# Kernel tuning notes

Hardware: AMD Instinct MI355X
Metric: run time of the kernel (lower is better)

## Reference

```python
import jax, jax.numpy as jnp
import numpy as np

B, T, C, H = 256, 256, 384, 64  # batch, seq (== block_size), n_embd, head_size


def setup_inputs() -> dict:
    key = jax.random.key(0)
    kx, kk, kq, kv = jax.random.split(key, 4)
    scale = C ** -0.5
    x = jax.random.normal(kx, (B, T, C), dtype=jnp.float32)
    Wk = jax.random.normal(kk, (C, H), dtype=jnp.float32) * scale
    Wq = jax.random.normal(kq, (C, H), dtype=jnp.float32) * scale
    Wv = jax.random.normal(kv, (C, H), dtype=jnp.float32) * scale
    return {"x": x, "Wk": Wk, "Wq": Wq, "Wv": Wv}


def reference(x, Wk, Wq, Wv):
    # Single causal self-attention head (x_kv=None path). Dropout is eval-mode (identity).
    Tn = x.shape[1]
    k = x @ Wk            # [B, T, H]
    q = x @ Wq            # [B, T, H]
    v = x @ Wv            # [B, T, H]
    inv_sqrt_d = k.shape[-1] ** -0.5
    wei = jnp.einsum('bth,bsh->bts', q, k) * inv_sqrt_d  # [B, T, T]
    causal = jnp.tril(jnp.ones((Tn, Tn), dtype=bool))
    wei = jnp.where(causal, wei, -jnp.inf)
    wei = jax.nn.softmax(wei, axis=-1)
    out = jnp.einsum('bts,bsh->bth', wei, v)             # [B, T, H]
    return out
```

## Files before the change

### kernel.cpp

```cpp
#include <hip/hip_runtime.h>

#define BATCH 256
#define SEQ   256
#define CDIM  384
#define HDIM  64

typedef __attribute__((ext_vector_type(8))) short bf16x8;
typedef __attribute__((ext_vector_type(4))) float f32x4;

__device__ __forceinline__ unsigned f2bf(float f) {
  union { float f; unsigned u; } v; v.f = f;
  unsigned r = v.u + 0x7FFFu + ((v.u >> 16) & 1u);
  return r >> 16;
}

__global__ void wtrans_kernel(const float* __restrict__ Wk, const float* __restrict__ Wq,
                              const float* __restrict__ Wv, unsigned short* __restrict__ WTf) {
  int gid = blockIdx.x * 256 + threadIdx.x;
  if (gid >= 192 * CDIM) return;
  int n = gid / CDIM, kk = gid - n * CDIM;
  const float* W = (n < 64) ? Wq : (n < 128) ? Wk : Wv;
  int nt = n >> 4, ln = n & 15, ks = kk >> 5, sub = (kk >> 3) & 3, j = kk & 7;
  int lane = ln + 16 * sub;
  WTf[(((size_t)ks * 12 + nt) * 64 + lane) * 8 + j] =
      (unsigned short)f2bf(W[kk * HDIM + (n & 63)]);
}

__global__ __launch_bounds__(512, 2) void proj_kernel(
    const float* __restrict__ x, const unsigned short* __restrict__ WTf,
    unsigned short* __restrict__ qws, unsigned short* __restrict__ kws,
    unsigned short* __restrict__ vT) {
  __shared__ unsigned short wtlds[73728];
  __shared__ unsigned short vtile[64][72];
  const int tid = threadIdx.x, bid = blockIdx.x;
  const int w = tid >> 6, lane = tid & 63;
  const int ln15 = lane & 15, quad = lane >> 4;

  {
    const uint4* src = (const uint4*)WTf;
    uint4* dst = (uint4*)wtlds;
    #pragma unroll
    for (int i = 0; i < 18; ++i) dst[i * 512 + tid] = src[i * 512 + tid];
  }

  const int t0 = bid * 128 + w * 16;
  const float* xrow = x + (size_t)(t0 + ln15) * CDIM + quad * 8;
  bf16x8 bx[12];
  #pragma unroll
  for (int hh = 0; hh < 2; ++hh) {
    float4 A[12];
    #pragma unroll
    for (int j = 0; j < 6; ++j) {
      A[2 * j]     = *(const float4*)(xrow + (hh * 6 + j) * 32);
      A[2 * j + 1] = *(const float4*)(xrow + (hh * 6 + j) * 32 + 4);
    }
    #pragma unroll
    for (int j = 0; j < 6; ++j) {
      bf16x8 t;
      t[0] = (short)f2bf(A[2 * j].x);     t[1] = (short)f2bf(A[2 * j].y);
      t[2] = (short)f2bf(A[2 * j].z);     t[3] = (short)f2bf(A[2 * j].w);
      t[4] = (short)f2bf(A[2 * j + 1].x); t[5] = (short)f2bf(A[2 * j + 1].y);
      t[6] = (short)f2bf(A[2 * j + 1].z); t[7] = (short)f2bf(A[2 * j + 1].w);
      bx[hh * 6 + j] = t;
    }
  }

  __syncthreads();

  f32x4 acc[12];
  #pragma unroll
  for (int nt = 0; nt < 12; ++nt) acc[nt] = (f32x4){0.f, 0.f, 0.f, 0.f};

  #pragma unroll
  for (int ks = 0; ks < 12; ++ks) {
    #pragma unroll
    for (int nt = 0; nt < 12; ++nt) {
      bf16x8 aw = *(const bf16x8*)&wtlds[((ks * 12 + nt) * 64 + lane) * 8];
      acc[nt] = __builtin_amdgcn_mfma_f32_16x16x32_bf16(aw, bx[ks], acc[nt], 0, 0, 0);
    }
  }

  #pragma unroll
  for (int nt = 0; nt < 8; ++nt) {
    unsigned p0 = f2bf(acc[nt][0]) | (f2bf(acc[nt][1]) << 16);
    unsigned p1 = f2bf(acc[nt][2]) | (f2bf(acc[nt][3]) << 16);
    int hl = (nt & 3) * 16 + quad * 4;
    unsigned short* dst = (nt < 4) ? qws : kws;
    *(uint2*)&dst[(size_t)(t0 + ln15) * HDIM + hl] = (uint2){p0, p1};
  }

  #pragma unroll
  for (int p = 0; p < 2; ++p) {
    if ((w >> 2) == p) {
      int tl = (w & 3) * 16 + ln15;
      #pragma unroll
      for (int nt = 8; nt < 12; ++nt) {
        int hl = (nt & 3) * 16 + quad * 4;
        #pragma unroll
        for (int i = 0; i < 4; ++i)
          vtile[hl + i][tl] = (unsigned short)f2bf(acc[nt][i]);
      }
    }
    __syncthreads();
    {
      int h = tid >> 3, c = tid & 7;
      uint4 d = *(const uint4*)&vtile[h][c * 8];
      *(uint4*)&vT[((size_t)(bid >> 1) * 64 + h) * SEQ + (bid & 1) * 128 + p * 64 + c * 8] = d;
    }
    __syncthreads();
  }
}

__global__ __launch_bounds__(512, 4) void attn_kernel(
    const unsigned short* __restrict__ qws, const unsigned short* __restrict__ kws,
    const unsigned short* __restrict__ vT, float* __restrict__ out) {
  __shared__ unsigned short kl[256][72];
  __shared__ unsigned short vt[64][264];
  __shared__ unsigned short pl[8][16][36];
  const int tid = threadIdx.x;
  const int b = blockIdx.x >> 1, hgrp = blockIdx.x & 1;
  const int w = tid >> 6, lane = tid & 63;
  const int ln15 = lane & 15, quad = lane >> 4;

  for (int c = tid; c < 2048; c += 512) {
    int t = c >> 3, hc = c & 7;
    *(uint4*)&kl[t][hc * 8] = *(const uint4*)&kws[(size_t)(b * 256 + t) * HDIM + hc * 8];
  }
  for (int c = tid; c < 2048; c += 512) {
    int hh = c >> 5, tc = c & 31;
    *(uint4*)&vt[hh][tc * 8] = *(const uint4*)&vT[(size_t)(b * 64 + hh) * SEQ + tc * 8];
  }
  __syncthreads();

  const int mt = 4 * (w >> 1) + (hgrp ? (1 + (w & 1)) : (3 * (w & 1)));
  const int t0 = mt * 16;
  const int NT = (mt | 1) + 1;

  bf16x8 aq[2];
  #pragma unroll
  for (int ks = 0; ks < 2; ++ks)
    aq[ks] = *(const bf16x8*)&qws[(size_t)(b * 256 + t0 + ln15) * HDIM + ks * 32 + quad * 8];

  float sv[16][4];
  #pragma unroll
  for (int nt = 0; nt < 16; ++nt) {
    if (nt < NT) {
      f32x4 acc = (f32x4){0.f, 0.f, 0.f, 0.f};
      #pragma unroll
      for (int ks = 0; ks < 2; ++ks) {
        bf16x8 bf = *(const bf16x8*)&kl[nt * 16 + ln15][ks * 32 + quad * 8];
        acc = __builtin_amdgcn_mfma_f32_16x16x32_bf16(aq[ks], bf, acc, 0, 0, 0);
      }
      int colg = nt * 16 + ln15;
      #pragma unroll
      for (int i = 0; i < 4; ++i) {
        int rowg = t0 + quad * 4 + i;
        sv[nt][i] = (colg <= rowg) ? acc[i] * 0.125f : -3.0e38f;
      }
    }
  }
  float mx[4] = {-3.0e38f, -3.0e38f, -3.0e38f, -3.0e38f};
  #pragma unroll
  for (int nt = 0; nt < 16; ++nt)
    if (nt < NT) {
      #pragma unroll
      for (int i = 0; i < 4; ++i) mx[i] = fmaxf(mx[i], sv[nt][i]);
    }
  #pragma unroll
  for (int i = 0; i < 4; ++i) {
    mx[i] = fmaxf(mx[i], __shfl_xor(mx[i], 8, 64));
    mx[i] = fmaxf(mx[i], __shfl_xor(mx[i], 4, 64));
    mx[i] = fmaxf(mx[i], __shfl_xor(mx[i], 2, 64));
    mx[i] = fmaxf(mx[i], __shfl_xor(mx[i], 1, 64));
  }
  float sm[4] = {0.f, 0.f, 0.f, 0.f};
  #pragma unroll
  for (int nt = 0; nt < 16; ++nt)
    if (nt < NT) {
      #pragma unroll
      for (int i = 0; i < 4; ++i) {
        float e = __expf(sv[nt][i] - mx[i]);
        sv[nt][i] = e;
        sm[i] += e;
      }
    }
  #pragma unroll
  for (int i = 0; i < 4; ++i) {
    sm[i] += __shfl_xor(sm[i], 8, 64);
    sm[i] += __shfl_xor(sm[i], 4, 64);
    sm[i] += __shfl_xor(sm[i], 2, 64);
    sm[i] += __shfl_xor(sm[i], 1, 64);
  }
  float inv[4];
  #pragma unroll
  for (int i = 0; i < 4; ++i) inv[i] = 1.0f / sm[i];

  f32x4 o[4];
  #pragma unroll
  for (int ont = 0; ont < 4; ++ont) o[ont] = (f32x4){0.f, 0.f, 0.f, 0.f};

  for (int kc = 0; kc < 8; ++kc) {
    if (kc * 2 < NT) {
      #pragma unroll
      for (int half = 0; half < 2; ++half) {
        int nt = kc * 2 + half;
        #pragma unroll
        for (int i = 0; i < 4; ++i)
          pl[w][quad * 4 + i][half * 16 + ln15] =
              (unsigned short)f2bf(sv[nt][i] * inv[i]);
      }
      bf16x8 pa = *(const bf16x8*)&pl[w][ln15][quad * 8];
      #pragma unroll
      for (int ont = 0; ont < 4; ++ont) {
        bf16x8 vb = *(const bf16x8*)&vt[ont * 16 + ln15][kc * 32 + quad * 8];
        o[ont] = __builtin_amdgcn_mfma_f32_16x16x32_bf16(pa, vb, o[ont], 0, 0, 0);
      }
    }
  }

  #pragma unroll
  for (int ont = 0; ont < 4; ++ont) {
    int h = ont * 16 + ln15;
    #pragma unroll
    for (int i = 0; i < 4; ++i)
      out[(size_t)(b * 256 + t0 + quad * 4 + i) * HDIM + h] = o[ont][i];
  }
}

extern "C" void kernel_launch(void* const* d_in, const int* in_sizes, int n_in,
                              void* d_out, int out_size, void* d_ws, size_t ws_size,
                              hipStream_t stream) {
  const float* x  = (const float*)d_in[0];
  const float* Wk = (const float*)d_in[1];
  const float* Wq = (const float*)d_in[2];
  const float* Wv = (const float*)d_in[3];
  float* out = (float*)d_out;

  char* ws = (char*)d_ws;
  unsigned short* WTf = (unsigned short*)ws;
  unsigned short* qws = (unsigned short*)(ws + 262144);
  unsigned short* kws = qws + (size_t)BATCH * SEQ * HDIM;
  unsigned short* vT  = kws + (size_t)BATCH * SEQ * HDIM;

  wtrans_kernel<<<(192 * CDIM + 255) / 256, 256, 0, stream>>>(Wk, Wq, Wv, WTf);
  proj_kernel<<<512, 512, 0, stream>>>(x, WTf, qws, kws, vT);
  attn_kernel<<<2 * BATCH, 512, 0, stream>>>(qws, kws, vT, out);
}
```

Before: 182.5 us.

## Fuse QKV projection and causal attention into one per-batch kernel

Merges the projection and attention kernels into one kernel with one block per batch. Each block computes Q, K and V for all 256 rows into shared memory, reusing the weight LDS region, then runs causal attention with each wave handling a short and a long row tile to balance the work. This removes the global round trip for bf16 Q/K/V and one kernel launch. In exchange the grid shrinks to 256 blocks, which risks lower occupancy and less latency hiding on a GPU with many CUs.

Result: slower. 190.0 us (+4.1%).

```diff
diff --git a/kernel.cpp b/kernel.cpp
--- a/kernel.cpp
+++ b/kernel.cpp
@@ -26,204 +26,196 @@
       (unsigned short)f2bf(W[kk * HDIM + (n & 63)]);
 }
 
-__global__ __launch_bounds__(512, 2) void proj_kernel(
+__global__ __launch_bounds__(512, 2) void fused_kernel(
     const float* __restrict__ x, const unsigned short* __restrict__ WTf,
-    unsigned short* __restrict__ qws, unsigned short* __restrict__ kws,
-    unsigned short* __restrict__ vT) {
-  __shared__ unsigned short wtlds[73728];
-  __shared__ unsigned short vtile[64][72];
-  const int tid = threadIdx.x, bid = blockIdx.x;
+    float* __restrict__ out) {
+  __shared__ unsigned short lds[73728];
+  const int tid = threadIdx.x, b = blockIdx.x;
   const int w = tid >> 6, lane = tid & 63;
   const int ln15 = lane & 15, quad = lane >> 4;
 
   {
     const uint4* src = (const uint4*)WTf;
-    uint4* dst = (uint4*)wtlds;
+    uint4* dst = (uint4*)lds;
     #pragma unroll
     for (int i = 0; i < 18; ++i) dst[i * 512 + tid] = src[i * 512 + tid];
   }
 
-  const int t0 = bid * 128 + w * 16;
-  const float* xrow = x + (size_t)(t0 + ln15) * CDIM + quad * 8;
-  bf16x8 bx[12];
+  bf16x8 bx[2][12];
+  {
+    const float* xr0 = x + (size_t)(b * 256 + w * 32 + ln15) * CDIM + quad * 8;
+    #pragma unroll
+    for (int rg = 0; rg < 2; ++rg) {
+      const float* xr = xr0 + rg * 16 * CDIM;
+      #pragma unroll
+      for (int hh = 0; hh < 2; ++hh) {
+        float4 A[12];
+        #pragma unroll
+        for (int j = 0; j < 6; ++j) {
+          A[2 * j]     = *(const float4*)(xr + (hh * 6 + j) * 32);
+          A[2 * j + 1] = *(const float4*)(xr + (hh * 6 + j) * 32 + 4);
+        }
+        #pragma unroll
+        for (int j = 0; j < 6; ++j) {
+          bf16x8 t;
+          t[0] = (short)f2bf(A[2 * j].x);     t[1] = (short)f2bf(A[2 * j].y);
+          t[2] = (short)f2bf(A[2 * j].z);     t[3] = (short)f2bf(A[2 * j].w);
+          t[4] = (short)f2bf(A[2 * j + 1].x); t[5] = (short)f2bf(A[2 * j + 1].y);
+          t[6] = (short)f2bf(A[2 * j + 1].z); t[7] = (short)f2bf(A[2 * j + 1].w);
+          bx[rg][hh * 6 + j] = t;
+        }
+      }
+    }
+  }
+
+  __syncthreads();
+
+  f32x4 acc[2][12];
   #pragma unroll
-  for (int hh = 0; hh < 2; ++hh) {
-    float4 A[12];
-    #pragma unroll
-    for (int j = 0; j < 6; ++j) {
-      A[2 * j]     = *(const float4*)(xrow + (hh * 6 + j) * 32);
-      A[2 * j + 1] = *(const float4*)(xrow + (hh * 6 + j) * 32 + 4);
-    }
-    #pragma unroll
-    for (int j = 0; j < 6; ++j) {
-      bf16x8 t;
-      t[0] = (short)f2bf(A[2 * j].x);     t[1] = (short)f2bf(A[2 * j].y);
-      t[2] = (short)f2bf(A[2 * j].z);     t[3] = (short)f2bf(A[2 * j].w);
-      t[4] = (short)f2bf(A[2 * j + 1].x); t[5] = (short)f2bf(A[2 * j + 1].y);
-      t[6] = (short)f2bf(A[2 * j + 1].z); t[7] = (short)f2bf(A[2 * j + 1].w);
-      bx[hh * 6 + j] = t;
-    }
-  }
-
-  __syncthreads();
-
-  f32x4 acc[12];
-  #pragma unroll
-  for (int nt = 0; nt < 12; ++nt) acc[nt] = (f32x4){0.f, 0.f, 0.f, 0.f};
+  for (int rg = 0; rg < 2; ++rg)
+    #pragma unroll
+    for (int nt = 0; nt < 12; ++nt) acc[rg][nt] = (f32x4){0.f, 0.f, 0.f, 0.f};
 
   #pragma unroll
   for (int ks = 0; ks < 12; ++ks) {
     #pragma unroll
     for (int nt = 0; nt < 12; ++nt) {
-      bf16x8 aw = *(const bf16x8*)&wtlds[((ks * 12 + nt) * 64 + lane) * 8];
-      acc[nt] = __builtin_amdgcn_mfma_f32_16x16x32_bf16(aw, bx[ks], acc[nt], 0, 0, 0);
-    }
-  }
+      bf16x8 aw = *(const bf16x8*)&lds[((ks * 12 + nt) * 64 + lane) * 8];
+      acc[0][nt] = __builtin_amdgcn_mfma_f32_16x16x32_bf16(aw, bx[0][ks], acc[0][nt], 0, 0, 0);
+      acc[1][nt] = __builtin_amdgcn_mfma_f32_16x16x32_bf16(aw, bx[1][ks], acc[1][nt], 0, 0, 0);
+    }
+  }
+
+  __syncthreads();
+
+  unsigned short (*QL)[72]  = (unsigned short(*)[72])lds;
+  unsigned short (*KL)[72]  = (unsigned short(*)[72])(lds + 18432);
+  unsigned short (*VT)[264] = (unsigned short(*)[264])(lds + 36864);
+  unsigned short (*PL)[36]  = (unsigned short(*)[36])(lds + 53760 + w * 576);
 
   #pragma unroll
-  for (int nt = 0; nt < 8; ++nt) {
-    unsigned p0 = f2bf(acc[nt][0]) | (f2bf(acc[nt][1]) << 16);
-    unsigned p1 = f2bf(acc[nt][2]) | (f2bf(acc[nt][3]) << 16);
-    int hl = (nt & 3) * 16 + quad * 4;
-    unsigned short* dst = (nt < 4) ? qws : kws;
-    *(uint2*)&dst[(size_t)(t0 + ln15) * HDIM + hl] = (uint2){p0, p1};
-  }
-
-  #pragma unroll
-  for (int p = 0; p < 2; ++p) {
-    if ((w >> 2) == p) {
-      int tl = (w & 3) * 16 + ln15;
+  for (int rg = 0; rg < 2; ++rg) {
+    const int trow = w * 32 + rg * 16 + ln15;
+    #pragma unroll
+    for (int nt = 0; nt < 4; ++nt) {
+      f32x4 a = acc[rg][nt];
+      unsigned p0 = f2bf(a[0]) | (f2bf(a[1]) << 16);
+      unsigned p1 = f2bf(a[2]) | (f2bf(a[3]) << 16);
+      *(uint2*)&QL[trow][nt * 16 + quad * 4] = (uint2){p0, p1};
+    }
+    #pragma unroll
+    for (int nt = 4; nt < 8; ++nt) {
+      f32x4 a = acc[rg][nt];
+      unsigned p0 = f2bf(a[0]) | (f2bf(a[1]) << 16);
+      unsigned p1 = f2bf(a[2]) | (f2bf(a[3]) << 16);
+      *(uint2*)&KL[trow][(nt - 4) * 16 + quad * 4] = (uint2){p0, p1};
+    }
+    #pragma unroll
+    for (int nt = 8; nt < 12; ++nt) {
+      f32x4 a = acc[rg][nt];
+      const int h = (nt - 8) * 16 + quad * 4;
       #pragma unroll
-      for (int nt = 8; nt < 12; ++nt) {
-        int hl = (nt & 3) * 16 + quad * 4;
-        #pragma unroll
-        for (int i = 0; i < 4; ++i)
-          vtile[hl + i][tl] = (unsigned short)f2bf(acc[nt][i]);
-      }
-    }
-    __syncthreads();
-    {
-      int h = tid >> 3, c = tid & 7;
-      uint4 d = *(const uint4*)&vtile[h][c * 8];
-      *(uint4*)&vT[((size_t)(bid >> 1) * 64 + h) * SEQ + (bid & 1) * 128 + p * 64 + c * 8] = d;
-    }
-    __syncthreads();
-  }
-}
-
-__global__ __launch_bounds__(512, 4) void attn_kernel(
-    const unsigned short* __restrict__ qws, const unsigned short* __restrict__ kws,
-    const unsigned short* __restrict__ vT, float* __restrict__ out) {
-  __shared__ unsigned short kl[256][72];
-  __shared__ unsigned short vt[64][264];
-  __shared__ unsigned short pl[8][16][36];
-  const int tid = threadIdx.x;
-  const int b = blockIdx.x >> 1, hgrp = blockIdx.x & 1;
-  const int w = tid >> 6, lane = tid & 63;
-  const int ln15 = lane & 15, quad = lane >> 4;
-
-  for (int c = tid; c < 2048; c += 512) {
-    int t = c >> 3, hc = c & 7;
-    *(uint4*)&kl[t][hc * 8] = *(const uint4*)&kws[(size_t)(b * 256 + t) * HDIM + hc * 8];
-  }
-  for (int c = tid; c < 2048; c += 512) {
-    int hh = c >> 5, tc = c & 31;
-    *(uint4*)&vt[hh][tc * 8] = *(const uint4*)&vT[(size_t)(b * 64 + hh) * SEQ + tc * 8];
+      for (int i = 0; i < 4; ++i)
+        VT[h + i][trow] = (unsigned short)f2bf(a[i]);
+    }
   }
   __syncthreads();
 
-  const int mt = 4 * (w >> 1) + (hgrp ? (1 + (w & 1)) : (3 * (w & 1)));
-  const int t0 = mt * 16;
-  const int NT = (mt | 1) + 1;
-
-  bf16x8 aq[2];
-  #pragma unroll
-  for (int ks = 0; ks < 2; ++ks)
-    aq[ks] = *(const bf16x8*)&qws[(size_t)(b * 256 + t0 + ln15) * HDIM + ks * 32 + quad * 8];
-
-  float sv[16][4];
-  #pragma unroll
-  for (int nt = 0; nt < 16; ++nt) {
-    if (nt < NT) {
-      f32x4 acc = (f32x4){0.f, 0.f, 0.f, 0.f};
+  for (int mi = 0; mi < 2; ++mi) {
+    const int mt = mi ? (15 - w) : w;
+    const int t0 = mt * 16;
+    const int NT = (mt | 1) + 1;
+
+    bf16x8 aq[2];
+    #pragma unroll
+    for (int ks = 0; ks < 2; ++ks)
+      aq[ks] = *(const bf16x8*)&QL[t0 + ln15][ks * 32 + quad * 8];
+
+    float sv[16][4];
+    #pragma unroll
+    for (int nt = 0; nt < 16; ++nt) {
+      if (nt < NT) {
+        f32x4 a2 = (f32x4){0.f, 0.f, 0.f, 0.f};
+        #pragma unroll
+        for (int ks = 0; ks < 2; ++ks) {
+          bf16x8 bf = *(const bf16x8*)&KL[nt * 16 + ln15][ks * 32 + quad * 8];
+          a2 = __builtin_amdgcn_mfma_f32_16x16x32_bf16(aq[ks], bf, a2, 0, 0, 0);
+        }
+        int colg = nt * 16 + ln15;
+        #pragma unroll
+        for (int i = 0; i < 4; ++i) {
+          int rowg = t0 + quad * 4 + i;
+          sv[nt][i] = (colg <= rowg) ? a2[i] * 0.125f : -3.0e38f;
+        }
+      }
+    }
+    float mx[4] = {-3.0e38f, -3.0e38f, -3.0e38f, -3.0e38f};
+    #pragma unroll
+    for (int nt = 0; nt < 16; ++nt)
+      if (nt < NT) {
+        #pragma unroll
+        for (int i = 0; i < 4; ++i) mx[i] = fmaxf(mx[i], sv[nt][i]);
+      }
+    #pragma unroll
+    for (int i = 0; i < 4; ++i) {
+      mx[i] = fmaxf(mx[i], __shfl_xor(mx[i], 8, 64));
+      mx[i] = fmaxf(mx[i], __shfl_xor(mx[i], 4, 64));
+      mx[i] = fmaxf(mx[i], __shfl_xor(mx[i], 2, 64));
+      mx[i] = fmaxf(mx[i], __shfl_xor(mx[i], 1, 64));
+    }
+    float sm[4] = {0.f, 0.f, 0.f, 0.f};
+    #pragma unroll
+    for (int nt = 0; nt < 16; ++nt)
+      if (nt < NT) {
+        #pragma unroll
+        for (int i = 0; i < 4; ++i) {
+          float e = __expf(sv[nt][i] - mx[i]);
+          sv[nt][i] = e;
+          sm[i] += e;
+        }
+      }
+    #pragma unroll
+    for (int i = 0; i < 4; ++i) {
+      sm[i] += __shfl_xor(sm[i], 8, 64);
+      sm[i] += __shfl_xor(sm[i], 4, 64);
+      sm[i] += __shfl_xor(sm[i], 2, 64);
+      sm[i] += __shfl_xor(sm[i], 1, 64);
+    }
+    float inv[4];
+    #pragma unroll
+    for (int i = 0; i < 4; ++i) inv[i] = 1.0f / sm[i];
+
+    f32x4 o[4];
+    #pragma unroll
+    for (int ont = 0; ont < 4; ++ont) o[ont] = (f32x4){0.f, 0.f, 0.f, 0.f};
+
+    #pragma unroll
+    for (int kc = 0; kc < 8; ++kc) {
+      if (kc * 2 < NT) {
+        #pragma unroll
+        for (int half = 0; half < 2; ++half) {
+          int nt = kc * 2 + half;
+          #pragma unroll
+          for (int i = 0; i < 4; ++i)
+            PL[quad * 4 + i][half * 16 + ln15] =
+                (unsigned short)f2bf(sv[nt][i] * inv[i]);
+        }
+        bf16x8 pa = *(const bf16x8*)&PL[ln15][quad * 8];
+        #pragma unroll
+        for (int ont = 0; ont < 4; ++ont) {
+          bf16x8 vb = *(const bf16x8*)&VT[ont * 16 + ln15][kc * 32 + quad * 8];
+          o[ont] = __builtin_amdgcn_mfma_f32_16x16x32_bf16(pa, vb, o[ont], 0, 0, 0);
+        }
+      }
+    }
+
+    #pragma unroll
+    for (int ont = 0; ont < 4; ++ont) {
+      int h = ont * 16 + ln15;
       #pragma unroll
-      for (int ks = 0; ks < 2; ++ks) {
-        bf16x8 bf = *(const bf16x8*)&kl[nt * 16 + ln15][ks * 32 + quad * 8];
-        acc = __builtin_amdgcn_mfma_f32_16x16x32_bf16(aq[ks], bf, acc, 0, 0, 0);
-      }
-      int colg = nt * 16 + ln15;
-      #pragma unroll
-      for (int i = 0; i < 4; ++i) {
-        int rowg = t0 + quad * 4 + i;
-        sv[nt][i] = (colg <= rowg) ? acc[i] * 0.125f : -3.0e38f;
-      }
-    }
-  }
-  float mx[4] = {-3.0e38f, -3.0e38f, -3.0e38f, -3.0e38f};
-  #pragma unroll
-  for (int nt = 0; nt < 16; ++nt)
-    if (nt < NT) {
-      #pragma unroll
-      for (int i = 0; i < 4; ++i) mx[i] = fmaxf(mx[i], sv[nt][i]);
-    }
-  #pragma unroll
-  for (int i = 0; i < 4; ++i) {
-    mx[i] = fmaxf(mx[i], __shfl_xor(mx[i], 8, 64));
-    mx[i] = fmaxf(mx[i], __shfl_xor(mx[i], 4, 64));
-    mx[i] = fmaxf(mx[i], __shfl_xor(mx[i], 2, 64));
-    mx[i] = fmaxf(mx[i], __shfl_xor(mx[i], 1, 64));
-  }
-  float sm[4] = {0.f, 0.f, 0.f, 0.f};
-  #pragma unroll
-  for (int nt = 0; nt < 16; ++nt)
-    if (nt < NT) {
-      #pragma unroll
-      for (int i = 0; i < 4; ++i) {
-        float e = __expf(sv[nt][i] - mx[i]);
-        sv[nt][i] = e;
-        sm[i] += e;
-      }
-    }
-  #pragma unroll
-  for (int i = 0; i < 4; ++i) {
-    sm[i] += __shfl_xor(sm[i], 8, 64);
-    sm[i] += __shfl_xor(sm[i], 4, 64);
-    sm[i] += __shfl_xor(sm[i], 2, 64);
-    sm[i] += __shfl_xor(sm[i], 1, 64);
-  }
-  float inv[4];
-  #pragma unroll
-  for (int i = 0; i < 4; ++i) inv[i] = 1.0f / sm[i];
-
-  f32x4 o[4];
-  #pragma unroll
-  for (int ont = 0; ont < 4; ++ont) o[ont] = (f32x4){0.f, 0.f, 0.f, 0.f};
-
-  for (int kc = 0; kc < 8; ++kc) {
-    if (kc * 2 < NT) {
-      #pragma unroll
-      for (int half = 0; half < 2; ++half) {
-        int nt = kc * 2 + half;
-        #pragma unroll
-        for (int i = 0; i < 4; ++i)
-          pl[w][quad * 4 + i][half * 16 + ln15] =
-              (unsigned short)f2bf(sv[nt][i] * inv[i]);
-      }
-      bf16x8 pa = *(const bf16x8*)&pl[w][ln15][quad * 8];
-      #pragma unroll
-      for (int ont = 0; ont < 4; ++ont) {
-        bf16x8 vb = *(const bf16x8*)&vt[ont * 16 + ln15][kc * 32 + quad * 8];
-        o[ont] = __builtin_amdgcn_mfma_f32_16x16x32_bf16(pa, vb, o[ont], 0, 0, 0);
-      }
-    }
-  }
-
-  #pragma unroll
-  for (int ont = 0; ont < 4; ++ont) {
-    int h = ont * 16 + ln15;
-    #pragma unroll
-    for (int i = 0; i < 4; ++i)
-      out[(size_t)(b * 256 + t0 + quad * 4 + i) * HDIM + h] = o[ont][i];
+      for (int i = 0; i < 4; ++i)
+        out[(size_t)(b * 256 + t0 + quad * 4 + i) * HDIM + h] = o[ont][i];
+    }
   }
 }
 
@@ -236,13 +228,8 @@
   const float* Wv = (const float*)d_in[3];
   float* out = (float*)d_out;
 
-  char* ws = (char*)d_ws;
-  unsigned short* WTf = (unsigned short*)ws;
-  unsigned short* qws = (unsigned short*)(ws + 262144);
-  unsigned short* kws = qws + (size_t)BATCH * SEQ * HDIM;
-  unsigned short* vT  = kws + (size_t)BATCH * SEQ * HDIM;
+  unsigned short* WTf = (unsigned short*)d_ws;
 
   wtrans_kernel<<<(192 * CDIM + 255) / 256, 256, 0, stream>>>(Wk, Wq, Wv, WTf);
-  proj_kernel<<<512, 512, 0, stream>>>(x, WTf, qws, kws, vT);
-  attn_kernel<<<2 * BATCH, 512, 0, stream>>>(qws, kws, vT, out);
-}
+  fused_kernel<<<256, 512, 0, stream>>>(x, WTf, out);
+}
```
